# Optimization experiments

Measured on AMD Instinct MI355X. Metric: run time of the kernel, lower is better.

The kernel has to match this reference:

```python
import jax, jax.numpy as jnp
import numpy as np

NUM_HOPS = 3

def _position_encoding(sentence_size, embedding_size):
    # Vectorized version of the double loop in the source.
    i = np.arange(1, embedding_size + 1, dtype=np.float32)[:, None]  # [E,1]
    j = np.arange(1, sentence_size + 1, dtype=np.float32)[None, :]   # [1,S]
    enc = (i - embedding_size / 2.0) * (j - sentence_size / 2.0)
    enc = 1.0 + 4.0 * enc / embedding_size / sentence_size
    return jnp.asarray(np.transpose(enc))  # [S, E]

def setup_inputs() -> dict:
    key = jax.random.key(0)
    ks = jax.random.split(key, 9)
    B, M, S, E, V, OUT = 16, 512, 32, 128, 32000, 128
    scale = 0.02
    return {
        "queries": jax.random.randint(ks[0], (B, S), 0, V, dtype=jnp.int32),
        "stories": jax.random.randint(ks[1], (B, M, S), 0, V, dtype=jnp.int32),
        "query_biases": jax.random.normal(ks[2], (V - 1, E), jnp.float32) * scale,
        "stories_biases": jax.random.normal(ks[3], (V - 1, E), jnp.float32) * scale,
        "memory_biases": jax.random.normal(ks[4], (M, E), jnp.float32) * scale,
        "output_biases": jax.random.normal(ks[5], (V - 1, E), jnp.float32) * scale,
        "w_intermediate": jax.random.normal(ks[6], (E, E), jnp.float32) * scale,
        "w_output": jax.random.normal(ks[7], (E, OUT), jnp.float32) * scale,
        "w_final": jax.random.normal(ks[8], (OUT, V), jnp.float32) * scale,
    }

def reference(queries, stories, query_biases, stories_biases, memory_biases,
              output_biases, w_intermediate, w_output, w_final):
    B, M, S = stories.shape
    E = query_biases.shape[1]
    enc = _position_encoding(S, E)  # [S, E]
    nil = jnp.zeros((1, E), dtype=query_biases.dtype)

    # Story memory: gather -> positional weight -> reduce over sentence axis.
    st_tab = jnp.concatenate([stories_biases, nil], axis=0)          # [V, E]
    mem_emb = st_tab[stories]                                        # [B,M,S,E]
    memory = jnp.einsum('bmse,se->bme', mem_emb, enc) + memory_biases

    # Query embedding.
    q_tab = jnp.concatenate([query_biases, nil], axis=0)
    q = jnp.einsum('bse,se->be', q_tab[queries], enc)                # [B,E]

    # Output memory.
    o_tab = jnp.concatenate([output_biases, nil], axis=0)
    output = jnp.einsum('bmse,se->bme', o_tab[stories], enc)         # [B,M,E]

    out_layer = q
    for hop in range(NUM_HOPS):
        probs = jax.nn.softmax(jnp.einsum('bme,be->bm', memory, q))  # [B,M]
        layer_out = jnp.einsum('bme,bm->be', output, probs)          # [B,E]
        w = w_output if hop == NUM_HOPS - 1 else w_intermediate
        out_layer = (q + layer_out) @ w
        q = out_layer                     # pre-nonlinearity state, as in source
        out_layer = jax.nn.relu(out_layer)

    return out_layer @ w_final            # [B, vocab]
```

## Files before the change

### kernel.cpp

```cpp
#include <hip/hip_runtime.h>

constexpr int kB  = 16;
constexpr int kM  = 512;
constexpr int kS  = 32;
constexpr int kE  = 128;
constexpr int kV  = 32000;
constexpr int kVN = kV - 1;
constexpr int kMS = 132;

__global__ __launch_bounds__(256) void embed_stories_kernel(
    const int*   __restrict__ stories,
    const float* __restrict__ st_bias,
    const float* __restrict__ out_bias,
    const float* __restrict__ mem_bias,
    float*       __restrict__ memory,
    float*       __restrict__ output,
    unsigned*    __restrict__ bar)
{
    __shared__ int sidx[2][kS];
    __shared__ __align__(16) float pm[8][kE];
    __shared__ __align__(16) float po[8][kE];

    const int t    = threadIdx.x;
    const int row0 = blockIdx.x * 2;
    if (t < 64) sidx[t >> 5][t & 31] = stories[row0 * kS + t];
    if (blockIdx.x == 0 && t < kB + 1) bar[t] = 0u;
    __syncthreads();

    const int g    = t >> 5;
    const int lane = t & 31;
    const int p    = g >> 2;
    const int ph   = g & 3;
    const int e0   = lane * 4;
    const float ef0 = (float)(e0 - 63), ef1 = (float)(e0 - 62);
    const float ef2 = (float)(e0 - 61), ef3 = (float)(e0 - 60);

    float4 am = {0.f, 0.f, 0.f, 0.f};
    float4 ao = {0.f, 0.f, 0.f, 0.f};
    #pragma unroll
    for (int j = 0; j < 8; ++j) {
        const int s   = ph * 8 + j;
        const int idx = sidx[p][s];
        const int ci  = idx < kVN ? idx : (kVN - 1);
        const float live = (idx < kVN) ? 1.0f : 0.0f;
        const float sf = (float)(s - 15) * (1.0f / 1024.0f);
        const float4 vm = *(const float4*)(st_bias  + (size_t)ci * kE + e0);
        const float4 vo = *(const float4*)(out_bias + (size_t)ci * kE + e0);
        const float c0 = fmaf(ef0, sf, 1.0f) * live;
        const float c1 = fmaf(ef1, sf, 1.0f) * live;
        const float c2 = fmaf(ef2, sf, 1.0f) * live;
        const float c3 = fmaf(ef3, sf, 1.0f) * live;
        am.x = fmaf(vm.x, c0, am.x); am.y = fmaf(vm.y, c1, am.y);
        am.z = fmaf(vm.z, c2, am.z); am.w = fmaf(vm.w, c3, am.w);
        ao.x = fmaf(vo.x, c0, ao.x); ao.y = fmaf(vo.y, c1, ao.y);
        ao.z = fmaf(vo.z, c2, ao.z); ao.w = fmaf(vo.w, c3, ao.w);
    }
    *(float4*)&pm[g][e0] = am;
    *(float4*)&po[g][e0] = ao;
    __syncthreads();

    const int pr = t >> 7;
    const int e  = t & 127;
    const int row = row0 + pr;
    const int m   = row & (kM - 1);
    const float sm = pm[pr * 4 + 0][e] + pm[pr * 4 + 1][e] +
                     pm[pr * 4 + 2][e] + pm[pr * 4 + 3][e];
    const float so = po[pr * 4 + 0][e] + po[pr * 4 + 1][e] +
                     po[pr * 4 + 2][e] + po[pr * 4 + 3][e];
    memory[(size_t)row * kE + e] = sm + mem_bias[m * kE + e];
    output[(size_t)row * kE + e] = so;
}

__device__ __forceinline__ void group_barrier(unsigned* ctr, unsigned target)
{
    __syncthreads();
    if (threadIdx.x == 0) {
        __hip_atomic_fetch_add(ctr, 1u, __ATOMIC_RELEASE, __HIP_MEMORY_SCOPE_AGENT);
        while (__hip_atomic_load(ctr, __ATOMIC_RELAXED, __HIP_MEMORY_SCOPE_AGENT) < target)
            __builtin_amdgcn_s_sleep(2);
    }
    __syncthreads();
}
__device__ __forceinline__ void cstore(float* p, float v) {
    __hip_atomic_store(p, v, __ATOMIC_RELAXED, __HIP_MEMORY_SCOPE_AGENT);
}
__device__ __forceinline__ float cload(const float* p) {
    return __hip_atomic_load(p, __ATOMIC_RELAXED, __HIP_MEMORY_SCOPE_AGENT);
}

__global__ __launch_bounds__(1024) void hops_final_kernel(
    const int*   __restrict__ queries,
    const float* __restrict__ q_bias,
    const float* __restrict__ memory,
    const float* __restrict__ output,
    const float* __restrict__ w_int,
    const float* __restrict__ w_out,
    const float* __restrict__ wf,
    float*       __restrict__ numer,
    float*       __restrict__ denom,
    float*                    xg,
    unsigned*    __restrict__ bar,
    float*       __restrict__ out)
{
    __shared__ __align__(16) float mem_lds[128 * kMS];
    __shared__ __align__(16) float out_lds[128 * kE];
    __shared__ float sc_q[128];
    __shared__ __align__(16) float q_s[kE];
    __shared__ float xb[kE];
    __shared__ __align__(16) float part8[8][kE];

    const int bid = blockIdx.x;
    const int b   = bid & 15;
    const int qtr = bid >> 4;
    const int t   = threadIdx.x;
    unsigned* ctr = bar + b;

    const float* memb = memory + ((size_t)b * kM + qtr * 128) * kE;
    const float* outb = output + ((size_t)b * kM + qtr * 128) * kE;
    #pragma unroll
    for (int i = 0; i < 4; ++i) {
        const int flat = t + i * 1024;
        const int rr = flat >> 5, ff = (flat & 31) * 4;
        *(float4*)&mem_lds[rr * kMS + ff] = *(const float4*)&memb[(size_t)rr * kE + ff];
        *(float4*)&out_lds[rr * kE  + ff] = *(const float4*)&outb[(size_t)rr * kE + ff];
    }

    if (t < 256) {
        const int g = t >> 5, lane = t & 31, e0 = lane * 4;
        const float f0 = (float)(e0 - 63) * (1.0f / 1024.0f);
        const float f1 = (float)(e0 - 62) * (1.0f / 1024.0f);
        const float f2 = (float)(e0 - 61) * (1.0f / 1024.0f);
        const float f3 = (float)(e0 - 60) * (1.0f / 1024.0f);
        float4 a = {0.f, 0.f, 0.f, 0.f};
        #pragma unroll
        for (int j = 0; j < 4; ++j) {
            const int s   = g * 4 + j;
            const int idx = queries[b * kS + s];
            const int ci  = idx < kVN ? idx : (kVN - 1);
            const float live = (idx < kVN) ? 1.0f : 0.0f;
            const float sf = (float)(s - 15);
            const float4 v = *(const float4*)&q_bias[(size_t)ci * kE + e0];
            a.x = fmaf(v.x, fmaf(f0, sf, 1.f) * live, a.x);
            a.y = fmaf(v.y, fmaf(f1, sf, 1.f) * live, a.y);
            a.z = fmaf(v.z, fmaf(f2, sf, 1.f) * live, a.z);
            a.w = fmaf(v.w, fmaf(f3, sf, 1.f) * live, a.w);
        }
        *(float4*)&part8[g][e0] = a;
    }
    __syncthreads();
    if (t < kE) {
        float s = 0.f;
        #pragma unroll
        for (int g = 0; g < 8; ++g) s += part8[g][t];
        q_s[t] = s;
    }
    __syncthreads();

    const int grp = t >> 7;
    const int e   = t & 127;

    for (int hop = 0; hop < 3; ++hop) {
        {
            const int rw = t >> 3, sub = t & 7;
            const float4* qv = (const float4*)&q_s[sub * 16];
            const float4* mv = (const float4*)&mem_lds[rw * kMS + sub * 16];
            float d = 0.f;
            #pragma unroll
            for (int i = 0; i < 4; ++i) {
                const float4 m4 = mv[i], q4 = qv[i];
                d = fmaf(m4.x, q4.x, d); d = fmaf(m4.y, q4.y, d);
                d = fmaf(m4.z, q4.z, d); d = fmaf(m4.w, q4.w, d);
            }
            d += __shfl_down(d, 4);
            d += __shfl_down(d, 2);
            d += __shfl_down(d, 1);
            if (sub == 0) sc_q[rw] = __expf(d);
        }
        __syncthreads();

        {
            float acc = 0.f;
            const float* pp = &sc_q[grp * 16];
            const float* ob = &out_lds[grp * 16 * kE + e];
            #pragma unroll
            for (int j = 0; j < 16; ++j)
                acc = fmaf(pp[j], ob[j * kE], acc);
            part8[grp][e] = acc;
        }
        __syncthreads();

        const int pb = hop & 1;
        float* nq = numer + (((size_t)pb * kB + b) * 4 + qtr) * kE;
        if (t < kE) {
            float s = 0.f;
            #pragma unroll
            for (int g = 0; g < 8; ++g) s += part8[g][t];
            cstore(&nq[t], s);
        } else if (t < 192) {
            const int l = t - 128;
            float s2 = sc_q[l] + sc_q[l + 64];
            #pragma unroll
            for (int off = 32; off; off >>= 1) s2 += __shfl_down(s2, off);
            if (l == 0) cstore(&denom[((size_t)pb * kB + b) * 4 + qtr], s2);
        }

        group_barrier(ctr, 4u * (hop + 1));

        if (t < kE) {
            const float* nn = numer + ((size_t)pb * kB + b) * 4 * kE;
            const float* dd = denom + ((size_t)pb * kB + b) * 4;
            const float ns = cload(&nn[t]) + cload(&nn[kE + t]) +
                             cload(&nn[2 * kE + t]) + cload(&nn[3 * kE + t]);
            const float ds = cload(&dd[0]) + cload(&dd[1]) +
                             cload(&dd[2]) + cload(&dd[3]);
            xb[t] = q_s[t] + ns / ds;
        }
        __syncthreads();

        {
            const float* w = (hop == 2) ? w_out : w_int;
            float acc = 0.f;
            #pragma unroll
            for (int j = 0; j < 16; ++j) {
                const int k = grp * 16 + j;
                acc = fmaf(xb[k], w[k * kE + e], acc);
            }
            part8[grp][e] = acc;
        }
        __syncthreads();
        if (t < kE) {
            float s = 0.f;
            #pragma unroll
            for (int g = 0; g < 8; ++g) s += part8[g][t];
            q_s[t] = s;
        }
        __syncthreads();
    }

    if (qtr == 0 && t < kE) cstore(&xg[t * kB + b], fmaxf(q_s[t], 0.f));
    group_barrier(bar + kB, 64u);

    float* sx = mem_lds;
    if (t < 512) {
        const float4 v4 = *(const float4*)&xg[t * 4];
        *(float4*)&sx[t * 4] = v4;
    }
    __syncthreads();

    {
        const int vt = t & 511;
        const int h  = t >> 9;
        const int v  = bid * 500 + vt;
        float* ps = out_lds;
        float acc[kB];
        #pragma unroll
        for (int b2 = 0; b2 < kB; ++b2) acc[b2] = 0.f;

        if (vt < 500) {
            const int e0 = h * 64;
            #pragma unroll 8
            for (int ei = 0; ei < 64; ++ei) {
                const int e = e0 + ei;
                const float wv = wf[(size_t)e * kV + v];
                const float* xr = &sx[e * kB];
                #pragma unroll
                for (int b2 = 0; b2 < kB; ++b2)
                    acc[b2] = fmaf(xr[b2], wv, acc[b2]);
            }
            if (h == 1) {
                #pragma unroll
                for (int b2 = 0; b2 < kB; ++b2) ps[b2 * 512 + vt] = acc[b2];
            }
        }
        __syncthreads();
        if (h == 0 && vt < 500) {
            #pragma unroll
            for (int b2 = 0; b2 < kB; ++b2)
                out[(size_t)b2 * kV + v] = acc[b2] + ps[b2 * 512 + vt];
        }
    }
}

extern "C" void kernel_launch(void* const* d_in, const int* in_sizes, int n_in,
                              void* d_out, int out_size, void* d_ws, size_t ws_size,
                              hipStream_t stream)
{
    const int*   queries  = (const int*)  d_in[0];
    const int*   stories  = (const int*)  d_in[1];
    const float* q_bias   = (const float*)d_in[2];
    const float* st_bias  = (const float*)d_in[3];
    const float* mem_bias = (const float*)d_in[4];
    const float* out_bias = (const float*)d_in[5];
    const float* w_int    = (const float*)d_in[6];
    const float* w_out    = (const float*)d_in[7];
    const float* w_final  = (const float*)d_in[8];
    float* out = (float*)d_out;

    float* memory = (float*)d_ws;
    float* output = memory + (size_t)kB * kM * kE;
    float* numer  = output + (size_t)kB * kM * kE;
    float* denom  = numer  + 2 * kB * 4 * kE;
    float* xg     = denom  + 2 * kB * 4;
    unsigned* bar = (unsigned*)(xg + kE * kB);

    embed_stories_kernel<<<dim3((kB * kM) / 2), dim3(256), 0, stream>>>(
        stories, st_bias, out_bias, mem_bias, memory, output, bar);

    hops_final_kernel<<<dim3(64), dim3(1024), 0, stream>>>(
        queries, q_bias, memory, output, w_int, w_out, w_final,
        numer, denom, xg, bar, out);
}
```

Measured before the change: 161.8 us.

## Split hop kernel across 256 blocks with 16 memory slices per batch

New measurement: 169.5 us. +4.8%, slower.

```diff
diff --git a/kernel.cpp b/kernel.cpp
--- a/kernel.cpp
+++ b/kernel.cpp
@@ -1,12 +1,14 @@
 #include <hip/hip_runtime.h>
 
-constexpr int kB  = 16;
-constexpr int kM  = 512;
-constexpr int kS  = 32;
-constexpr int kE  = 128;
-constexpr int kV  = 32000;
-constexpr int kVN = kV - 1;
-constexpr int kMS = 132;
+constexpr int kB    = 16;
+constexpr int kM    = 512;
+constexpr int kS    = 32;
+constexpr int kE    = 128;
+constexpr int kV    = 32000;
+constexpr int kVN   = kV - 1;
+constexpr int kMS   = 132;
+constexpr int kQ    = 16;
+constexpr int kRows = kM / kQ;
 
 __global__ __launch_bounds__(256) void embed_stories_kernel(
     const int*   __restrict__ stories,
@@ -102,12 +104,16 @@
     unsigned*    __restrict__ bar,
     float*       __restrict__ out)
 {
-    __shared__ __align__(16) float mem_lds[128 * kMS];
-    __shared__ __align__(16) float out_lds[128 * kE];
-    __shared__ float sc_q[128];
+    constexpr int kPS  = 7 * 128 * 17;
+    constexpr int kPool = kPS + kE * kB;
+    __shared__ __align__(16) float pool[kPool];
+    __shared__ __align__(16) float part8[8][kE];
+    __shared__ float sc_q[kRows];
     __shared__ __align__(16) float q_s[kE];
     __shared__ float xb[kE];
-    __shared__ __align__(16) float part8[8][kE];
+
+    float* mem_lds = pool;
+    float* out_lds = pool + kRows * kMS;
 
     const int bid = blockIdx.x;
     const int b   = bid & 15;
@@ -115,14 +121,13 @@
     const int t   = threadIdx.x;
     unsigned* ctr = bar + b;
 
-    const float* memb = memory + ((size_t)b * kM + qtr * 128) * kE;
-    const float* outb = output + ((size_t)b * kM + qtr * 128) * kE;
-    #pragma unroll
-    for (int i = 0; i < 4; ++i) {
-        const int flat = t + i * 1024;
-        const int rr = flat >> 5, ff = (flat & 31) * 4;
-        *(float4*)&mem_lds[rr * kMS + ff] = *(const float4*)&memb[(size_t)rr * kE + ff];
-        *(float4*)&out_lds[rr * kE  + ff] = *(const float4*)&outb[(size_t)rr * kE + ff];
+    {
+        const size_t base = ((size_t)b * kM + qtr * kRows) * kE;
+        const int rr = t >> 5, ff = (t & 31) * 4;
+        *(float4*)&mem_lds[rr * kMS + ff] =
+            *(const float4*)&memory[base + (size_t)rr * kE + ff];
+        *(float4*)&out_lds[rr * kE  + ff] =
+            *(const float4*)&output[base + (size_t)rr * kE + ff];
     }
 
     if (t < 256) {
@@ -156,68 +161,67 @@
     }
     __syncthreads();
 
-    const int grp = t >> 7;
-    const int e   = t & 127;
-
     for (int hop = 0; hop < 3; ++hop) {
         {
-            const int rw = t >> 3, sub = t & 7;
-            const float4* qv = (const float4*)&q_s[sub * 16];
-            const float4* mv = (const float4*)&mem_lds[rw * kMS + sub * 16];
+            const int rw = t >> 5, sub = t & 31;
+            const float4 q4 = ((const float4*)q_s)[sub];
+            const float4 m4 = *(const float4*)&mem_lds[rw * kMS + sub * 4];
             float d = 0.f;
-            #pragma unroll
-            for (int i = 0; i < 4; ++i) {
-                const float4 m4 = mv[i], q4 = qv[i];
-                d = fmaf(m4.x, q4.x, d); d = fmaf(m4.y, q4.y, d);
-                d = fmaf(m4.z, q4.z, d); d = fmaf(m4.w, q4.w, d);
-            }
-            d += __shfl_down(d, 4);
-            d += __shfl_down(d, 2);
-            d += __shfl_down(d, 1);
+            d = fmaf(m4.x, q4.x, d); d = fmaf(m4.y, q4.y, d);
+            d = fmaf(m4.z, q4.z, d); d = fmaf(m4.w, q4.w, d);
+            d += __shfl_down(d, 16, 32);
+            d += __shfl_down(d, 8, 32);
+            d += __shfl_down(d, 4, 32);
+            d += __shfl_down(d, 2, 32);
+            d += __shfl_down(d, 1, 32);
             if (sub == 0) sc_q[rw] = __expf(d);
         }
         __syncthreads();
 
         {
+            const int grp = t >> 7, e = t & 127;
             float acc = 0.f;
-            const float* pp = &sc_q[grp * 16];
-            const float* ob = &out_lds[grp * 16 * kE + e];
-            #pragma unroll
-            for (int j = 0; j < 16; ++j)
-                acc = fmaf(pp[j], ob[j * kE], acc);
+            #pragma unroll
+            for (int j = 0; j < 4; ++j)
+                acc = fmaf(sc_q[grp * 4 + j], out_lds[(grp * 4 + j) * kE + e], acc);
             part8[grp][e] = acc;
         }
         __syncthreads();
 
         const int pb = hop & 1;
-        float* nq = numer + (((size_t)pb * kB + b) * 4 + qtr) * kE;
+        float* nq = numer + (((size_t)pb * kB + b) * kQ + qtr) * kE;
         if (t < kE) {
             float s = 0.f;
             #pragma unroll
             for (int g = 0; g < 8; ++g) s += part8[g][t];
             cstore(&nq[t], s);
-        } else if (t < 192) {
+        } else if (t < 160) {
             const int l = t - 128;
-            float s2 = sc_q[l] + sc_q[l + 64];
-            #pragma unroll
-            for (int off = 32; off; off >>= 1) s2 += __shfl_down(s2, off);
-            if (l == 0) cstore(&denom[((size_t)pb * kB + b) * 4 + qtr], s2);
-        }
-
-        group_barrier(ctr, 4u * (hop + 1));
+            float s2 = sc_q[l];
+            s2 += __shfl_down(s2, 16, 32);
+            s2 += __shfl_down(s2, 8, 32);
+            s2 += __shfl_down(s2, 4, 32);
+            s2 += __shfl_down(s2, 2, 32);
+            s2 += __shfl_down(s2, 1, 32);
+            if (l == 0) cstore(&denom[((size_t)pb * kB + b) * kQ + qtr], s2);
+        }
+
+        group_barrier(ctr, (unsigned)kQ * (hop + 1));
 
         if (t < kE) {
-            const float* nn = numer + ((size_t)pb * kB + b) * 4 * kE;
-            const float* dd = denom + ((size_t)pb * kB + b) * 4;
-            const float ns = cload(&nn[t]) + cload(&nn[kE + t]) +
-                             cload(&nn[2 * kE + t]) + cload(&nn[3 * kE + t]);
-            const float ds = cload(&dd[0]) + cload(&dd[1]) +
-                             cload(&dd[2]) + cload(&dd[3]);
+            const float* nn = numer + ((size_t)pb * kB + b) * kQ * kE;
+            const float* dd = denom + ((size_t)pb * kB + b) * kQ;
+            float ns = 0.f, ds = 0.f;
+            #pragma unroll
+            for (int j = 0; j < kQ; ++j) ns += cload(&nn[j * kE + t]);
+            #pragma unroll
+            for (int j = 0; j < kQ; ++j) ds += cload(&dd[j]);
             xb[t] = q_s[t] + ns / ds;
         }
         __syncthreads();
 
         {
+            const int grp = t >> 7, e = t & 127;
             const float* w = (hop == 2) ? w_out : w_int;
             float acc = 0.f;
             #pragma unroll
@@ -238,28 +242,27 @@
     }
 
     if (qtr == 0 && t < kE) cstore(&xg[t * kB + b], fmaxf(q_s[t], 0.f));
-    group_barrier(bar + kB, 64u);
-
-    float* sx = mem_lds;
+    group_barrier(bar + kB, 256u);
+
+    float* ps = pool;
+    float* sx = pool + kPS;
     if (t < 512) {
-        const float4 v4 = *(const float4*)&xg[t * 4];
-        *(float4*)&sx[t * 4] = v4;
+        *(float4*)&sx[t * 4] = *(const float4*)&xg[t * 4];
     }
     __syncthreads();
 
     {
-        const int vt = t & 511;
-        const int h  = t >> 9;
-        const int v  = bid * 500 + vt;
-        float* ps = out_lds;
+        const int vt = t & 127;
+        const int h  = t >> 7;
+        const int v  = bid * 125 + vt;
         float acc[kB];
         #pragma unroll
         for (int b2 = 0; b2 < kB; ++b2) acc[b2] = 0.f;
 
-        if (vt < 500) {
-            const int e0 = h * 64;
-            #pragma unroll 8
-            for (int ei = 0; ei < 64; ++ei) {
+        if (vt < 125) {
+            const int e0 = h * 16;
+            #pragma unroll
+            for (int ei = 0; ei < 16; ++ei) {
                 const int e = e0 + ei;
                 const float wv = wf[(size_t)e * kV + v];
                 const float* xr = &sx[e * kB];
@@ -267,16 +270,22 @@
                 for (int b2 = 0; b2 < kB; ++b2)
                     acc[b2] = fmaf(xr[b2], wv, acc[b2]);
             }
-            if (h == 1) {
+            if (h > 0) {
                 #pragma unroll
-                for (int b2 = 0; b2 < kB; ++b2) ps[b2 * 512 + vt] = acc[b2];
+                for (int b2 = 0; b2 < kB; ++b2)
+                    ps[(h - 1) * (128 * 17) + vt * 17 + b2] = acc[b2];
             }
         }
         __syncthreads();
-        if (h == 0 && vt < 500) {
-            #pragma unroll
-            for (int b2 = 0; b2 < kB; ++b2)
-                out[(size_t)b2 * kV + v] = acc[b2] + ps[b2 * 512 + vt];
+        if (h == 0 && vt < 125) {
+            #pragma unroll
+            for (int b2 = 0; b2 < kB; ++b2) {
+                float s = acc[b2];
+                #pragma unroll
+                for (int j = 0; j < 7; ++j)
+                    s += ps[j * (128 * 17) + vt * 17 + b2];
+                out[(size_t)b2 * kV + v] = s;
+            }
         }
     }
 }
@@ -299,14 +308,14 @@
     float* memory = (float*)d_ws;
     float* output = memory + (size_t)kB * kM * kE;
     float* numer  = output + (size_t)kB * kM * kE;
-    float* denom  = numer  + 2 * kB * 4 * kE;
-    float* xg     = denom  + 2 * kB * 4;
+    float* denom  = numer  + 2 * kB * kQ * kE;
+    float* xg     = denom  + 2 * kB * kQ;
     unsigned* bar = (unsigned*)(xg + kE * kB);
 
     embed_stories_kernel<<<dim3((kB * kM) / 2), dim3(256), 0, stream>>>(
         stories, st_bias, out_bias, mem_bias, memory, output, bar);
 
-    hops_final_kernel<<<dim3(64), dim3(1024), 0, stream>>>(
+    hops_final_kernel<<<dim3(256), dim3(1024), 0, stream>>>(
         queries, q_bias, memory, output, w_int, w_out, w_final,
         numer, denom, xg, bar, out);
 }
```

## Replace final global barrier with per-batch flags and single-block last-hop projection

Applied to the files above, without the earlier changes.

Result: slower. 173.6 us (+7.3%).

```diff
diff --git a/kernel.cpp b/kernel.cpp
--- a/kernel.cpp
+++ b/kernel.cpp
@@ -1,12 +1,12 @@
 #include <hip/hip_runtime.h>
 
-constexpr int kB  = 16;
-constexpr int kM  = 512;
-constexpr int kS  = 32;
-constexpr int kE  = 128;
-constexpr int kV  = 32000;
-constexpr int kVN = kV - 1;
-constexpr int kMS = 132;
+constexpr int kB    = 16;
+constexpr int kM    = 512;
+constexpr int kS    = 32;
+constexpr int kE    = 128;
+constexpr int kV    = 32000;
+constexpr int kVN   = kV - 1;
+constexpr int kMS   = 132;
 
 __global__ __launch_bounds__(256) void embed_stories_kernel(
     const int*   __restrict__ stories,
@@ -24,7 +24,7 @@
     const int t    = threadIdx.x;
     const int row0 = blockIdx.x * 2;
     if (t < 64) sidx[t >> 5][t & 31] = stories[row0 * kS + t];
-    if (blockIdx.x == 0 && t < kB + 1) bar[t] = 0u;
+    if (blockIdx.x == 0 && t < 32) bar[t] = 0u;
     __syncthreads();
 
     const int g    = t >> 5;
@@ -98,8 +98,8 @@
     const float* __restrict__ wf,
     float*       __restrict__ numer,
     float*       __restrict__ denom,
-    float*                    xg,
-    unsigned*    __restrict__ bar,
+    float*                    sxg,
+    unsigned*                 bar,
     float*       __restrict__ out)
 {
     __shared__ __align__(16) float mem_lds[128 * kMS];
@@ -107,7 +107,7 @@
     __shared__ float sc_q[128];
     __shared__ __align__(16) float q_s[kE];
     __shared__ float xb[kE];
-    __shared__ __align__(16) float part8[8][kE];
+    __shared__ float dtmp;
 
     const int bid = blockIdx.x;
     const int b   = bid & 15;
@@ -125,39 +125,41 @@
         *(float4*)&out_lds[rr * kE  + ff] = *(const float4*)&outb[(size_t)rr * kE + ff];
     }
 
-    if (t < 256) {
-        const int g = t >> 5, lane = t & 31, e0 = lane * 4;
-        const float f0 = (float)(e0 - 63) * (1.0f / 1024.0f);
-        const float f1 = (float)(e0 - 62) * (1.0f / 1024.0f);
-        const float f2 = (float)(e0 - 61) * (1.0f / 1024.0f);
-        const float f3 = (float)(e0 - 60) * (1.0f / 1024.0f);
-        float4 a = {0.f, 0.f, 0.f, 0.f};
-        #pragma unroll
-        for (int j = 0; j < 4; ++j) {
-            const int s   = g * 4 + j;
-            const int idx = queries[b * kS + s];
-            const int ci  = idx < kVN ? idx : (kVN - 1);
-            const float live = (idx < kVN) ? 1.0f : 0.0f;
-            const float sf = (float)(s - 15);
-            const float4 v = *(const float4*)&q_bias[(size_t)ci * kE + e0];
-            a.x = fmaf(v.x, fmaf(f0, sf, 1.f) * live, a.x);
-            a.y = fmaf(v.y, fmaf(f1, sf, 1.f) * live, a.y);
-            a.z = fmaf(v.z, fmaf(f2, sf, 1.f) * live, a.z);
-            a.w = fmaf(v.w, fmaf(f3, sf, 1.f) * live, a.w);
-        }
-        *(float4*)&part8[g][e0] = a;
-    }
-    __syncthreads();
-    if (t < kE) {
-        float s = 0.f;
-        #pragma unroll
-        for (int g = 0; g < 8; ++g) s += part8[g][t];
-        q_s[t] = s;
-    }
-    __syncthreads();
-
-    const int grp = t >> 7;
-    const int e   = t & 127;
+    {
+        __shared__ __align__(16) float part8q[8][kE];
+        if (t < 256) {
+            const int g = t >> 5, lane = t & 31, e0 = lane * 4;
+            const float f0 = (float)(e0 - 63) * (1.0f / 1024.0f);
+            const float f1 = (float)(e0 - 62) * (1.0f / 1024.0f);
+            const float f2 = (float)(e0 - 61) * (1.0f / 1024.0f);
+            const float f3 = (float)(e0 - 60) * (1.0f / 1024.0f);
+            float4 a = {0.f, 0.f, 0.f, 0.f};
+            #pragma unroll
+            for (int j = 0; j < 4; ++j) {
+                const int s   = g * 4 + j;
+                const int idx = queries[b * kS + s];
+                const int ci  = idx < kVN ? idx : (kVN - 1);
+                const float live = (idx < kVN) ? 1.0f : 0.0f;
+                const float sf = (float)(s - 15);
+                const float4 v = *(const float4*)&q_bias[(size_t)ci * kE + e0];
+                a.x = fmaf(v.x, fmaf(f0, sf, 1.f) * live, a.x);
+                a.y = fmaf(v.y, fmaf(f1, sf, 1.f) * live, a.y);
+                a.z = fmaf(v.z, fmaf(f2, sf, 1.f) * live, a.z);
+                a.w = fmaf(v.w, fmaf(f3, sf, 1.f) * live, a.w);
+            }
+            *(float4*)&part8q[g][e0] = a;
+        }
+        __syncthreads();
+        if (t < kE) {
+            float s = 0.f;
+            #pragma unroll
+            for (int g = 0; g < 8; ++g) s += part8q[g][t];
+            q_s[t] = s;
+        }
+        __syncthreads();
+    }
+
+    __shared__ __align__(16) float part8[8][kE];
 
     for (int hop = 0; hop < 3; ++hop) {
         {
@@ -179,6 +181,7 @@
         __syncthreads();
 
         {
+            const int grp = t >> 7, e = t & 127;
             float acc = 0.f;
             const float* pp = &sc_q[grp * 16];
             const float* ob = &out_lds[grp * 16 * kE + e];
@@ -204,46 +207,95 @@
             if (l == 0) cstore(&denom[((size_t)pb * kB + b) * 4 + qtr], s2);
         }
 
-        group_barrier(ctr, 4u * (hop + 1));
-
-        if (t < kE) {
-            const float* nn = numer + ((size_t)pb * kB + b) * 4 * kE;
-            const float* dd = denom + ((size_t)pb * kB + b) * 4;
-            const float ns = cload(&nn[t]) + cload(&nn[kE + t]) +
-                             cload(&nn[2 * kE + t]) + cload(&nn[3 * kE + t]);
-            const float ds = cload(&dd[0]) + cload(&dd[1]) +
-                             cload(&dd[2]) + cload(&dd[3]);
-            xb[t] = q_s[t] + ns / ds;
-        }
-        __syncthreads();
-
-        {
-            const float* w = (hop == 2) ? w_out : w_int;
-            float acc = 0.f;
-            #pragma unroll
-            for (int j = 0; j < 16; ++j) {
-                const int k = grp * 16 + j;
-                acc = fmaf(xb[k], w[k * kE + e], acc);
-            }
-            part8[grp][e] = acc;
-        }
-        __syncthreads();
-        if (t < kE) {
-            float s = 0.f;
-            #pragma unroll
-            for (int g = 0; g < 8; ++g) s += part8[g][t];
-            q_s[t] = s;
-        }
-        __syncthreads();
-    }
-
-    if (qtr == 0 && t < kE) cstore(&xg[t * kB + b], fmaxf(q_s[t], 0.f));
-    group_barrier(bar + kB, 64u);
+        if (hop < 2) {
+            group_barrier(ctr, 4u * (hop + 1));
+
+            if (t < kE) {
+                const float* nn = numer + ((size_t)pb * kB + b) * 4 * kE;
+                const float* dd = denom + ((size_t)pb * kB + b) * 4;
+                const float ns = cload(&nn[t]) + cload(&nn[kE + t]) +
+                                 cload(&nn[2 * kE + t]) + cload(&nn[3 * kE + t]);
+                const float ds = cload(&dd[0]) + cload(&dd[1]) +
+                                 cload(&dd[2]) + cload(&dd[3]);
+                xb[t] = q_s[t] + ns / ds;
+            }
+            __syncthreads();
+
+            {
+                const int grp = t >> 7, e = t & 127;
+                float acc = 0.f;
+                #pragma unroll
+                for (int j = 0; j < 16; ++j) {
+                    const int k = grp * 16 + j;
+                    acc = fmaf(xb[k], w_int[k * kE + e], acc);
+                }
+                part8[grp][e] = acc;
+            }
+            __syncthreads();
+            if (t < kE) {
+                float s = 0.f;
+                #pragma unroll
+                for (int g = 0; g < 8; ++g) s += part8[g][t];
+                q_s[t] = s;
+            }
+            __syncthreads();
+        } else {
+            __syncthreads();
+            if (t == 0)
+                __hip_atomic_fetch_add(ctr, 1u, __ATOMIC_RELEASE,
+                                       __HIP_MEMORY_SCOPE_AGENT);
+            if (qtr == 0) {
+                if (t == 0) {
+                    while (__hip_atomic_load(ctr, __ATOMIC_RELAXED,
+                                             __HIP_MEMORY_SCOPE_AGENT) < 12u)
+                        __builtin_amdgcn_s_sleep(2);
+                }
+                __syncthreads();
+                if (t < kE) {
+                    const float* nn = numer + ((size_t)pb * kB + b) * 4 * kE;
+                    const float* dd = denom + ((size_t)pb * kB + b) * 4;
+                    const float ns = cload(&nn[t]) + cload(&nn[kE + t]) +
+                                     cload(&nn[2 * kE + t]) + cload(&nn[3 * kE + t]);
+                    const float ds = cload(&dd[0]) + cload(&dd[1]) +
+                                     cload(&dd[2]) + cload(&dd[3]);
+                    xb[t] = q_s[t] + ns / ds;
+                }
+                __syncthreads();
+                {
+                    const int grp = t >> 7, e = t & 127;
+                    float acc = 0.f;
+                    #pragma unroll
+                    for (int j = 0; j < 16; ++j) {
+                        const int k = grp * 16 + j;
+                        acc = fmaf(xb[k], w_out[k * kE + e], acc);
+                    }
+                    part8[grp][e] = acc;
+                }
+                __syncthreads();
+                if (t < kE) {
+                    float s = 0.f;
+                    #pragma unroll
+                    for (int g = 0; g < 8; ++g) s += part8[g][t];
+                    cstore(&sxg[b * kE + t], fmaxf(s, 0.f));
+                }
+                __syncthreads();
+                if (t == 0)
+                    __hip_atomic_store(&bar[16 + b], 1u, __ATOMIC_RELEASE,
+                                       __HIP_MEMORY_SCOPE_AGENT);
+            }
+        }
+    }
+
+    if (t < 16) {
+        while (__hip_atomic_load(&bar[16 + t], __ATOMIC_RELAXED,
+                                 __HIP_MEMORY_SCOPE_AGENT) == 0u)
+            __builtin_amdgcn_s_sleep(2);
+    }
+    __syncthreads();
 
     float* sx = mem_lds;
     if (t < 512) {
-        const float4 v4 = *(const float4*)&xg[t * 4];
-        *(float4*)&sx[t * 4] = v4;
+        *(float4*)&sx[t * 4] = *(const float4*)&sxg[t * 4];
     }
     __syncthreads();
 
@@ -262,10 +314,9 @@
             for (int ei = 0; ei < 64; ++ei) {
                 const int e = e0 + ei;
                 const float wv = wf[(size_t)e * kV + v];
-                const float* xr = &sx[e * kB];
                 #pragma unroll
                 for (int b2 = 0; b2 < kB; ++b2)
-                    acc[b2] = fmaf(xr[b2], wv, acc[b2]);
+                    acc[b2] = fmaf(sx[b2 * kE + e], wv, acc[b2]);
             }
             if (h == 1) {
                 #pragma unroll
@@ -300,13 +351,13 @@
     float* output = memory + (size_t)kB * kM * kE;
     float* numer  = output + (size_t)kB * kM * kE;
     float* denom  = numer  + 2 * kB * 4 * kE;
-    float* xg     = denom  + 2 * kB * 4;
-    unsigned* bar = (unsigned*)(xg + kE * kB);
+    float* sxg    = denom  + 2 * kB * 4;
+    unsigned* bar = (unsigned*)(sxg + kB * kE);
 
     embed_stories_kernel<<<dim3((kB * kM) / 2), dim3(256), 0, stream>>>(
         stories, st_bias, out_bias, mem_bias, memory, output, bar);
 
     hops_final_kernel<<<dim3(64), dim3(1024), 0, stream>>>(
         queries, q_bias, memory, output, w_int, w_out, w_final,
-        numer, denom, xg, bar, out);
-}
+        numer, denom, sxg, bar, out);
+}
```
